# Optimization experiments

Measured on AMD Instinct MI355X. Metric: run time of the kernel, lower is better.

The kernel has to match this reference:

```python
import jax, jax.numpy as jnp
import numpy as np
from jax import lax

IN_FEATURES = 1024
NUM_TAGS = 128
C = NUM_TAGS + 3          # CRF adds start/stop (+1 pad slot per original code)
START_IDX = C - 2
STOP_IDX = C - 1
NEG = -10000.0


def setup_inputs() -> dict:
    key = jax.random.key(0)
    k1, k2, k3, k4 = jax.random.split(key, 4)
    B, L = 64, 512
    x = jax.random.normal(k1, (B, L, IN_FEATURES), dtype=jnp.float32)
    mask = jnp.ones((B, L), dtype=jnp.float32)
    W = jax.random.normal(k2, (C, IN_FEATURES), dtype=jnp.float32) * (1.0 / np.sqrt(IN_FEATURES))
    b = jax.random.normal(k3, (C,), dtype=jnp.float32) * 0.01
    transitions = jax.random.normal(k4, (C, C), dtype=jnp.float32)
    # transitions[i, j] = score of transitioning FROM j TO i
    transitions = transitions.at[START_IDX, :].set(NEG)   # never transition into start
    transitions = transitions.at[:, STOP_IDX].set(NEG)    # never transition out of stop
    return {"x": x, "mask": mask, "W": W, "b": b, "transitions": transitions}


def reference(x, mask, W, b, transitions):
    """CRF forward: linear projection + Viterbi decode.
    Returns (best_score [B], best_paths [B, L])."""
    feats = jnp.einsum("bld,cd->blc", x, W) + b          # [B, L, C]
    B, L, Cn = feats.shape

    init_score = jnp.full((B, Cn), NEG, dtype=feats.dtype).at[:, START_IDX].set(0.0)

    def viterbi_step(score, inp):
        feat_t, mask_t = inp                              # [B, C], [B]
        # acc[b, i, j] = score[b, j] + transitions[i, j]
        acc = score[:, None, :] + transitions[None, :, :]  # [B, C, C]
        best = jnp.max(acc, axis=-1)                      # [B, C]
        bp = jnp.argmax(acc, axis=-1).astype(jnp.int32)   # [B, C]
        m = mask_t[:, None]
        new_score = (best + feat_t) * m + score * (1.0 - m)
        return new_score, bp

    final_score, bps = lax.scan(
        viterbi_step, init_score,
        (jnp.transpose(feats, (1, 0, 2)), mask.T))        # bps: [L, B, C]

    final_score = final_score + transitions[STOP_IDX]     # [B, C]
    best_score = jnp.max(final_score, axis=-1)            # [B]
    best_tag = jnp.argmax(final_score, axis=-1).astype(jnp.int32)  # [B]

    def backtrack(tag, bp_t):
        # tag: current tag at timestep t; bp_t: [B, C] backpointers at t
        prev = jnp.take_along_axis(bp_t, tag[:, None], axis=1)[:, 0]
        return prev, tag                                  # emit tag at timestep t

    _, path = lax.scan(backtrack, best_tag, bps, reverse=True)  # path: [L, B]
    best_paths = path.T                                   # [B, L]
    return best_score, best_paths
```

## Files before the change

### kernel.cpp

```cpp
#include <hip/hip_runtime.h>

#define BB 64
#define LL 512
#define DD 1024
#define CC 131
#define CP 132
#define START_I 129
#define STOP_I 130
#define NEGV -10000.0f

__device__ __forceinline__ void lds_barrier() {
    asm volatile("s_waitcnt lgkmcnt(0)" ::: "memory");
    __builtin_amdgcn_s_barrier();
    __builtin_amdgcn_sched_barrier(0);
}

#define RL(src, i) __int_as_float(__builtin_amdgcn_readlane(__float_as_int(src), (i)))

#define GM 64
#define GK 32
#define LSTR 36

__global__ __launch_bounds__(256, 2) void gemm_feats(
    const float* __restrict__ x, const float* __restrict__ W,
    const float* __restrict__ bias, float* __restrict__ feats)
{
    __shared__ float xs[GM * LSTR];
    __shared__ float ws[CP * LSTR];

    const int tid = threadIdx.x;
    const int m0 = blockIdx.x * GM;
    const int tm = tid & 15;
    const int tj = (tid >> 4) & 15;
    const bool tail = (tj < 3);
    const int tjt = (tj < 3) ? tj : 2;

    float acc[4][8];
    float acct[4];
#pragma unroll
    for (int r = 0; r < 4; ++r) {
        acct[r] = 0.f;
#pragma unroll
        for (int c = 0; c < 8; ++c) acc[r][c] = 0.f;
    }

    for (int kc = 0; kc < DD / GK; ++kc) {
        const int k0 = kc * GK;
        if (kc) __syncthreads();
#pragma unroll
        for (int q = 0; q < 2; ++q) {
            int lin = tid + q * 256;
            int m = lin >> 3, c4 = lin & 7;
            float4 v = *(const float4*)&x[(size_t)(m0 + m) * DD + k0 + c4 * 4];
            *(float4*)&xs[m * LSTR + c4 * 4] = v;
        }
#pragma unroll
        for (int q = 0; q < 5; ++q) {
            int lin = tid + q * 256;
            if (lin < CC * 8) {
                int r = lin >> 3, c4 = lin & 7;
                float4 v = *(const float4*)&W[(size_t)r * DD + k0 + c4 * 4];
                *(float4*)&ws[r * LSTR + c4 * 4] = v;
            }
        }
        __syncthreads();

#pragma unroll
        for (int k4 = 0; k4 < 8; ++k4) {
            float4 xr[4], wr[8], wt;
#pragma unroll
            for (int r = 0; r < 4; ++r)
                xr[r] = *(const float4*)&xs[(tm + 16 * r) * LSTR + k4 * 4];
#pragma unroll
            for (int c = 0; c < 8; ++c)
                wr[c] = *(const float4*)&ws[(tj + 16 * c) * LSTR + k4 * 4];
            wt = *(const float4*)&ws[(128 + tjt) * LSTR + k4 * 4];
#pragma unroll
            for (int r = 0; r < 4; ++r) {
#pragma unroll
                for (int c = 0; c < 8; ++c) {
                    acc[r][c] = fmaf(xr[r].x, wr[c].x, acc[r][c]);
                    acc[r][c] = fmaf(xr[r].y, wr[c].y, acc[r][c]);
                    acc[r][c] = fmaf(xr[r].z, wr[c].z, acc[r][c]);
                    acc[r][c] = fmaf(xr[r].w, wr[c].w, acc[r][c]);
                }
                acct[r] = fmaf(xr[r].x, wt.x, acct[r]);
                acct[r] = fmaf(xr[r].y, wt.y, acct[r]);
                acct[r] = fmaf(xr[r].z, wt.z, acct[r]);
                acct[r] = fmaf(xr[r].w, wt.w, acct[r]);
            }
        }
    }

#pragma unroll
    for (int c = 0; c < 8; ++c) {
        int j = tj + 16 * c;
        float bv = bias[j];
#pragma unroll
        for (int r = 0; r < 4; ++r)
            feats[(size_t)(m0 + tm + 16 * r) * CP + j] = acc[r][c] + bv;
    }
    if (tail) {
        int j = 128 + tj;
        float bv = bias[j];
#pragma unroll
        for (int r = 0; r < 4; ++r)
            feats[(size_t)(m0 + tm + 16 * r) * CP + j] = acct[r] + bv;
    }
}

__global__ __launch_bounds__(192, 1) void viterbi_fwd(
    const float* __restrict__ feats, const float* __restrict__ mask,
    const float* __restrict__ trans, float* __restrict__ hist)
{
    const int b = blockIdx.x;
    const int tid = threadIdx.x;
    const int wave = tid >> 6, lane = tid & 63;
    const int colc = (wave < 2) ? (wave * 64 + lane)
                                : (128 + ((lane < 2) ? lane : 2));
    const bool owner = (wave < 2) || (lane < 3);

    __shared__ float sbuf[2][132];

    float4 T[33];
    {
        const float* tr = trans + (size_t)colc * CC;
#pragma unroll
        for (int q = 0; q < 32; ++q) {
            T[q].x = tr[4 * q + 0]; T[q].y = tr[4 * q + 1];
            T[q].z = tr[4 * q + 2]; T[q].w = tr[4 * q + 3];
        }
        T[32].x = tr[128]; T[32].y = tr[129]; T[32].z = tr[130];
        T[32].w = NEGV;
    }
#pragma unroll
    for (int q = 0; q < 33; ++q)
        asm volatile("" : "+v"(T[q].x), "+v"(T[q].y), "+v"(T[q].z), "+v"(T[q].w));

    for (int q = tid; q < 2 * 132; q += 192) {
        int bufi = q / 132, idx = q - bufi * 132;
        sbuf[bufi][idx] = (bufi == 0 && idx == START_I) ? 0.f : NEGV;
    }
    __syncthreads();

    const float* fb = feats + (size_t)b * LL * CP;
    const float* mb = mask + (size_t)b * LL;
    float* hb = hist + (size_t)b * LL * CP;

    float s_reg = (colc == START_I) ? 0.f : NEGV;

    float fv0 = fb[colc], fv1 = fb[CP + colc];
    float mv0 = mb[0], mv1 = mb[1];
    const float* fb_t = fb + 2 * CP + colc;
    const float* mb_t = mb + 2;
    float* hb_t = hb + colc;

    int cur = 0;
    float ns_p = 0.f;

    for (int t = 0; t < LL; ++t) {
        if (t > 0) {
            if (owner) *hb_t = ns_p;
            hb_t += CP;
        }
        float fv2 = 0.f, mv2 = 1.f;
        if (t + 2 < LL) { fv2 = *fb_t; mv2 = *mb_t; }
        fb_t += CP; ++mb_t;

        float sa = sbuf[cur][lane];
        float sb = sbuf[cur][64 + lane];
        float s128 = sbuf[cur][128], s129 = sbuf[cur][129], s130 = sbuf[cur][130];

        float a0 = -3.0e38f, a1 = -3.0e38f, a2 = -3.0e38f, a3 = -3.0e38f;
#pragma unroll
        for (int q = 0; q < 16; ++q) {
            float4 t4 = T[q];
            a0 = fmaxf(fmaxf(RL(sa, 4 * q + 0) + t4.x, RL(sa, 4 * q + 1) + t4.y), a0);
            a1 = fmaxf(fmaxf(RL(sa, 4 * q + 2) + t4.z, RL(sa, 4 * q + 3) + t4.w), a1);
        }
#pragma unroll
        for (int q = 0; q < 16; ++q) {
            float4 t4 = T[16 + q];
            a2 = fmaxf(fmaxf(RL(sb, 4 * q + 0) + t4.x, RL(sb, 4 * q + 1) + t4.y), a2);
            a3 = fmaxf(fmaxf(RL(sb, 4 * q + 2) + t4.z, RL(sb, 4 * q + 3) + t4.w), a3);
        }
        {
            float4 t4 = T[32];
            a0 = fmaxf(fmaxf(s128 + t4.x, s129 + t4.y), a0);
            a1 = fmaxf(a1, s130 + t4.z);
        }
        float best = fmaxf(fmaxf(a0, a1), fmaxf(a2, a3));

        float ns = (mv0 != 0.f) ? (best + fv0) : s_reg;
        s_reg = ns;
        if (owner) sbuf[cur ^ 1][colc] = ns;
        ns_p = ns;

        lds_barrier();

        fv0 = fv1; fv1 = fv2; mv0 = mv1; mv1 = mv2;
        cur ^= 1;
    }
    if (owner) *hb_t = ns_p;
}

__global__ __launch_bounds__(256, 4) void bp_kernel(
    const float* __restrict__ hist, const float* __restrict__ trans,
    unsigned char* __restrict__ bp)
{
    const int b  = blockIdx.x / 5;
    const int jc = blockIdx.x % 5;
    const int tc = blockIdx.y;
    const int tid = threadIdx.x;
    const int j0 = jc * 32;

    __shared__ float Ts[32][136];
    __shared__ float hs[8][132];

    for (int q = 0; q < 17; ++q) {
        int lin = tid + q * 256;
        if (lin < 32 * CC) {
            int r = lin / CC, i = lin - r * CC;
            if (j0 + r < CC) Ts[r][i] = trans[(size_t)(j0 + r) * CC + i];
        }
    }
    {
        const float4* src = (const float4*)(hist + ((size_t)b * LL + tc * 8) * CP);
#pragma unroll
        for (int q = 0; q < 2; ++q) {
            int lin = tid + q * 256;
            if (lin < (8 * CP) / 4) ((float4*)hs)[lin] = src[lin];
        }
    }
    __syncthreads();

    const int jl = tid & 31;
    const int tt = tid >> 5;
    const int j = j0 + jl;
    const int t = tc * 8 + tt + 1;
    if (j >= CC || t >= LL) return;

    float best; int idx;
    {
        float4 tv = *(const float4*)&Ts[jl][128];
        float4 hv = *(const float4*)&hs[tt][128];
        best = hv.z + tv.z; idx = 130;
        float v;
        v = hv.y + tv.y; if (v >= best) { best = v; idx = 129; }
        v = hv.x + tv.x; if (v >= best) { best = v; idx = 128; }
    }
#pragma unroll
    for (int i4 = 31; i4 >= 0; --i4) {
        float4 tv = *(const float4*)&Ts[jl][i4 * 4];
        float4 hv = *(const float4*)&hs[tt][i4 * 4];
        float v;
        v = hv.w + tv.w; if (v >= best) { best = v; idx = i4 * 4 + 3; }
        v = hv.z + tv.z; if (v >= best) { best = v; idx = i4 * 4 + 2; }
        v = hv.y + tv.y; if (v >= best) { best = v; idx = i4 * 4 + 1; }
        v = hv.x + tv.x; if (v >= best) { best = v; idx = i4 * 4 + 0; }
    }
    bp[((size_t)b * LL + t) * CP + j] = (unsigned char)idx;
}

__global__ __launch_bounds__(64, 1) void viterbi_btr(
    const float* __restrict__ hist, const float* __restrict__ trans,
    const unsigned char* __restrict__ bp,
    float* __restrict__ out_score, float* __restrict__ out_path)
{
    const int b = blockIdx.x;
    const int lane = threadIdx.x;
    const float* hb = hist + ((size_t)b * LL + (LL - 1)) * CP;
    const float* ts = trans + (size_t)STOP_I * CC;

    float v0 = hb[lane] + ts[lane];
    float v1 = hb[lane + 64] + ts[lane + 64];
    float v2 = (lane < 3) ? (hb[lane + 128] + ts[lane + 128]) : -3.0e38f;

    float best = v0; int idx = lane;
    if (v1 > best) { best = v1; idx = lane + 64; }
    if (v2 > best) { best = v2; idx = lane + 128; }
#pragma unroll
    for (int off = 32; off >= 1; off >>= 1) {
        float ob = __shfl_xor(best, off, 64);
        int   oi = __shfl_xor(idx, off, 64);
        if (ob > best || (ob == best && oi < idx)) { best = ob; idx = oi; }
    }

    float* op = out_path + (size_t)b * LL;
    if (lane == 0) {
        out_score[b] = best;
        op[LL - 1] = (float)idx;
    }
    int tag = idx;

    __shared__ unsigned char buf[2][1088];
    const unsigned char* bpb = bp + (size_t)b * LL * CP;

    {
        const unsigned int* src = (const unsigned int*)(bpb + (size_t)504 * CP);
        unsigned int* dst = (unsigned int*)buf[1];
#pragma unroll
        for (int q = 0; q < 5; ++q) {
            int lin = lane + q * 64;
            if (lin < 264) dst[lin] = src[lin];
        }
    }
    lds_barrier();

    int cur = 1;
    for (int k = 63; k >= 0; --k) {
        unsigned int r0 = 0, r1 = 0, r2 = 0, r3 = 0, r4 = 0;
        if (k > 0) {
            const unsigned int* src = (const unsigned int*)(bpb + (size_t)(k - 1) * 8 * CP);
            r0 = src[lane];
            r1 = src[lane + 64];
            r2 = src[lane + 128];
            r3 = src[lane + 192];
            if (lane < 8) r4 = src[lane + 256];
        }
        const unsigned char* cb = buf[cur];
#pragma unroll
        for (int s = 7; s >= 0; --s) {
            int t = k * 8 + s;
            if (t >= 1) {
                tag = cb[s * CP + tag];
                if (lane == 0) op[t - 1] = (float)tag;
            }
        }
        if (k > 0) {
            unsigned int* dst = (unsigned int*)buf[cur ^ 1];
            dst[lane] = r0;
            dst[lane + 64] = r1;
            dst[lane + 128] = r2;
            dst[lane + 192] = r3;
            if (lane < 8) dst[lane + 256] = r4;
            lds_barrier();
        }
        cur ^= 1;
    }
}

extern "C" void kernel_launch(void* const* d_in, const int* in_sizes, int n_in,
                              void* d_out, int out_size, void* d_ws, size_t ws_size,
                              hipStream_t stream)
{
    const float* x     = (const float*)d_in[0];
    const float* mask  = (const float*)d_in[1];
    const float* W     = (const float*)d_in[2];
    const float* bias  = (const float*)d_in[3];
    const float* trans = (const float*)d_in[4];

    float* feats = (float*)d_ws;
    float* hist  = feats + (size_t)BB * LL * CP;
    unsigned char* bp = (unsigned char*)(hist + (size_t)BB * LL * CP);
    float* out_score = (float*)d_out;
    float* out_path  = out_score + BB;

    hipLaunchKernelGGL(gemm_feats, dim3((BB * LL) / GM), dim3(256), 0, stream, x, W, bias, feats);
    hipLaunchKernelGGL(viterbi_fwd, dim3(BB), dim3(192), 0, stream, feats, mask, trans, hist);
    hipLaunchKernelGGL(bp_kernel, dim3(BB * 5, 64), dim3(256), 0, stream, hist, trans, bp);
    hipLaunchKernelGGL(viterbi_btr, dim3(BB), dim3(64), 0, stream, hist, trans, bp, out_score, out_path);
}
```

Baseline: 732.6 us.

## Split Viterbi forward max over source-state halves across four waves

```diff
diff --git a/kernel.cpp b/kernel.cpp
--- a/kernel.cpp
+++ b/kernel.cpp
@@ -109,99 +109,145 @@
     }
 }
 
-__global__ __launch_bounds__(192, 1) void viterbi_fwd(
+__global__ __launch_bounds__(256, 1) void viterbi_fwd(
     const float* __restrict__ feats, const float* __restrict__ mask,
     const float* __restrict__ trans, float* __restrict__ hist)
 {
     const int b = blockIdx.x;
     const int tid = threadIdx.x;
     const int wave = tid >> 6, lane = tid & 63;
-    const int colc = (wave < 2) ? (wave * 64 + lane)
-                                : (128 + ((lane < 2) ? lane : 2));
-    const bool owner = (wave < 2) || (lane < 3);
-
-    __shared__ float sbuf[2][132];
-
-    float4 T[33];
+    const int h  = wave >> 1;
+    const int jg = wave & 1;
+    const int j  = jg * 64 + lane;
+    const int c  = h * 64 + lane;
+
+    __shared__ float pbuf[2][2][132];
+    __shared__ float tpbuf[2][3][2];
+
+    float4 T[17];
     {
-        const float* tr = trans + (size_t)colc * CC;
-#pragma unroll
-        for (int q = 0; q < 32; ++q) {
+        const float* tr = trans + (size_t)j * CC + h * 64;
+#pragma unroll
+        for (int q = 0; q < 16; ++q) {
             T[q].x = tr[4 * q + 0]; T[q].y = tr[4 * q + 1];
             T[q].z = tr[4 * q + 2]; T[q].w = tr[4 * q + 3];
         }
-        T[32].x = tr[128]; T[32].y = tr[129]; T[32].z = tr[130];
-        T[32].w = NEGV;
-    }
-#pragma unroll
-    for (int q = 0; q < 33; ++q)
+        if (h == 0) {
+            T[16] = make_float4(NEGV, NEGV, NEGV, NEGV);
+        } else {
+            T[16].x = tr[64]; T[16].y = tr[65]; T[16].z = tr[66];
+            T[16].w = NEGV;
+        }
+    }
+#pragma unroll
+    for (int q = 0; q < 17; ++q)
         asm volatile("" : "+v"(T[q].x), "+v"(T[q].y), "+v"(T[q].z), "+v"(T[q].w));
 
-    for (int q = tid; q < 2 * 132; q += 192) {
-        int bufi = q / 132, idx = q - bufi * 132;
-        sbuf[bufi][idx] = (bufi == 0 && idx == START_I) ? 0.f : NEGV;
-    }
-    __syncthreads();
+    const int tjA = (jg == 0) ? 128 : 130;
+    const bool hasB = (jg == 0);
+    float ttA = trans[(size_t)tjA * CC + h * 64 + lane];
+    float ttB = hasB ? trans[(size_t)129 * CC + h * 64 + lane] : NEGV;
+    float ttxA = NEGV, ttxB = NEGV;
+    if (h == 1 && lane < 3) {
+        ttxA = trans[(size_t)tjA * CC + 128 + lane];
+        if (hasB) ttxB = trans[(size_t)129 * CC + 128 + lane];
+    }
 
     const float* fb = feats + (size_t)b * LL * CP;
     const float* mb = mask + (size_t)b * LL;
     float* hb = hist + (size_t)b * LL * CP;
 
-    float s_reg = (colc == START_I) ? 0.f : NEGV;
-
-    float fv0 = fb[colc], fv1 = fb[CP + colc];
+    float  sa = NEGV;
+    float4 sv = make_float4(NEGV, 0.f, NEGV, NEGV);
+    float  st = (lane == 1) ? 0.f : NEGV;
+
+    const bool tl = (h == 1 && lane < 3);
+
+    float fv0 = fb[c], fv1 = fb[CP + c];
     float mv0 = mb[0], mv1 = mb[1];
-    const float* fb_t = fb + 2 * CP + colc;
-    const float* mb_t = mb + 2;
-    float* hb_t = hb + colc;
+    float ft0 = 0.f, ft1 = 0.f;
+    if (tl) { ft0 = fb[128 + lane]; ft1 = fb[CP + 128 + lane]; }
+    const float* fb_t  = fb + 2 * CP + c;
+    const float* ftb_t = fb + 2 * CP + 128 + lane;
+    const float* mb_t  = mb + 2;
 
     int cur = 0;
-    float ns_p = 0.f;
-
     for (int t = 0; t < LL; ++t) {
-        if (t > 0) {
-            if (owner) *hb_t = ns_p;
-            hb_t += CP;
-        }
-        float fv2 = 0.f, mv2 = 1.f;
-        if (t + 2 < LL) { fv2 = *fb_t; mv2 = *mb_t; }
-        fb_t += CP; ++mb_t;
-
-        float sa = sbuf[cur][lane];
-        float sb = sbuf[cur][64 + lane];
-        float s128 = sbuf[cur][128], s129 = sbuf[cur][129], s130 = sbuf[cur][130];
+        float fv2 = 0.f, mv2 = 1.f, ft2 = 0.f;
+        if (t + 2 < LL) { fv2 = *fb_t; mv2 = *mb_t; if (tl) ft2 = *ftb_t; }
+        fb_t += CP; ftb_t += CP; ++mb_t;
 
         float a0 = -3.0e38f, a1 = -3.0e38f, a2 = -3.0e38f, a3 = -3.0e38f;
 #pragma unroll
-        for (int q = 0; q < 16; ++q) {
+        for (int q = 0; q < 8; ++q) {
             float4 t4 = T[q];
             a0 = fmaxf(fmaxf(RL(sa, 4 * q + 0) + t4.x, RL(sa, 4 * q + 1) + t4.y), a0);
             a1 = fmaxf(fmaxf(RL(sa, 4 * q + 2) + t4.z, RL(sa, 4 * q + 3) + t4.w), a1);
         }
 #pragma unroll
-        for (int q = 0; q < 16; ++q) {
-            float4 t4 = T[16 + q];
-            a2 = fmaxf(fmaxf(RL(sb, 4 * q + 0) + t4.x, RL(sb, 4 * q + 1) + t4.y), a2);
-            a3 = fmaxf(fmaxf(RL(sb, 4 * q + 2) + t4.z, RL(sb, 4 * q + 3) + t4.w), a3);
-        }
+        for (int q = 8; q < 16; ++q) {
+            float4 t4 = T[q];
+            a2 = fmaxf(fmaxf(RL(sa, 4 * q + 0) + t4.x, RL(sa, 4 * q + 1) + t4.y), a2);
+            a3 = fmaxf(fmaxf(RL(sa, 4 * q + 2) + t4.z, RL(sa, 4 * q + 3) + t4.w), a3);
+        }
+        if (h == 1) {
+            float4 t4 = T[16];
+            a0 = fmaxf(fmaxf(sv.x + t4.x, sv.y + t4.y), a0);
+            a1 = fmaxf(fmaxf(sv.z + t4.z, sv.w + t4.w), a1);
+        }
+        float p = fmaxf(fmaxf(a0, a1), fmaxf(a2, a3));
+        pbuf[cur][h][j] = p;
+
         {
-            float4 t4 = T[32];
-            a0 = fmaxf(fmaxf(s128 + t4.x, s129 + t4.y), a0);
-            a1 = fmaxf(a1, s130 + t4.z);
-        }
-        float best = fmaxf(fmaxf(a0, a1), fmaxf(a2, a3));
-
-        float ns = (mv0 != 0.f) ? (best + fv0) : s_reg;
-        s_reg = ns;
-        if (owner) sbuf[cur ^ 1][colc] = ns;
-        ns_p = ns;
+            float cA = sa + ttA;
+            if (h == 1 && lane < 3) {
+                float svl = (lane == 0) ? sv.x : ((lane == 1) ? sv.y : sv.z);
+                cA = fmaxf(cA, svl + ttxA);
+            }
+#pragma unroll
+            for (int off = 1; off < 64; off <<= 1)
+                cA = fmaxf(cA, __shfl_xor(cA, off, 64));
+            if (lane == 0) tpbuf[cur][tjA - 128][h] = cA;
+            if (hasB) {
+                float cB = sa + ttB;
+                if (h == 1 && lane < 3) {
+                    float svl = (lane == 0) ? sv.x : ((lane == 1) ? sv.y : sv.z);
+                    cB = fmaxf(cB, svl + ttxB);
+                }
+#pragma unroll
+                for (int off = 1; off < 64; off <<= 1)
+                    cB = fmaxf(cB, __shfl_xor(cB, off, 64));
+                if (lane == 0) tpbuf[cur][1][h] = cB;
+            }
+        }
 
         lds_barrier();
 
-        fv0 = fv1; fv1 = fv2; mv0 = mv1; mv1 = mv2;
+        {
+            float best = fmaxf(pbuf[cur][0][c], pbuf[cur][1][c]);
+            float ns = (mv0 != 0.f) ? (best + fv0) : sa;
+            sa = ns;
+            if (wave == 0 || wave == 2) hb[(size_t)t * CP + c] = ns;
+        }
+        if (h == 1) {
+            float2 u0 = *(const float2*)&tpbuf[cur][0][0];
+            float2 u1 = *(const float2*)&tpbuf[cur][1][0];
+            float2 u2 = *(const float2*)&tpbuf[cur][2][0];
+            float c128 = fmaxf(u0.x, u0.y);
+            float c129 = fmaxf(u1.x, u1.y);
+            float c130 = fmaxf(u2.x, u2.y);
+            if (lane < 3) {
+                float comb = (lane == 0) ? c128 : ((lane == 1) ? c129 : c130);
+                float nst = (mv0 != 0.f) ? (comb + ft0) : st;
+                st = nst;
+                if (wave == 3) hb[(size_t)t * CP + 128 + lane] = nst;
+            }
+            sv.x = RL(st, 0); sv.y = RL(st, 1); sv.z = RL(st, 2); sv.w = NEGV;
+        }
+
+        fv0 = fv1; fv1 = fv2; mv0 = mv1; mv1 = mv2; ft0 = ft1; ft1 = ft2;
         cur ^= 1;
     }
-    if (owner) *hb_t = ns_p;
 }
 
 __global__ __launch_bounds__(256, 4) void bp_kernel(
@@ -357,7 +403,7 @@
     float* out_path  = out_score + BB;
 
     hipLaunchKernelGGL(gemm_feats, dim3((BB * LL) / GM), dim3(256), 0, stream, x, W, bias, feats);
-    hipLaunchKernelGGL(viterbi_fwd, dim3(BB), dim3(192), 0, stream, feats, mask, trans, hist);
+    hipLaunchKernelGGL(viterbi_fwd, dim3(BB), dim3(256), 0, stream, feats, mask, trans, hist);
     hipLaunchKernelGGL(bp_kernel, dim3(BB * 5, 64), dim3(256), 0, stream, hist, trans, bp);
     hipLaunchKernelGGL(viterbi_btr, dim3(BB), dim3(64), 0, stream, hist, trans, bp, out_score, out_path);
 }
```

After: 833.0 us. +13.7%, slower.

## Split Viterbi forward max across four waves plus dedicated tail wave

Applied to the files above, without the earlier changes.

```diff
diff --git a/kernel.cpp b/kernel.cpp
--- a/kernel.cpp
+++ b/kernel.cpp
@@ -109,99 +109,190 @@
     }
 }
 
-__global__ __launch_bounds__(192, 1) void viterbi_fwd(
+__global__ __launch_bounds__(320, 1) void viterbi_fwd(
     const float* __restrict__ feats, const float* __restrict__ mask,
     const float* __restrict__ trans, float* __restrict__ hist)
 {
     const int b = blockIdx.x;
     const int tid = threadIdx.x;
     const int wave = tid >> 6, lane = tid & 63;
-    const int colc = (wave < 2) ? (wave * 64 + lane)
-                                : (128 + ((lane < 2) ? lane : 2));
-    const bool owner = (wave < 2) || (lane < 3);
-
-    __shared__ float sbuf[2][132];
-
-    float4 T[33];
-    {
-        const float* tr = trans + (size_t)colc * CC;
-#pragma unroll
-        for (int q = 0; q < 32; ++q) {
-            T[q].x = tr[4 * q + 0]; T[q].y = tr[4 * q + 1];
-            T[q].z = tr[4 * q + 2]; T[q].w = tr[4 * q + 3];
-        }
-        T[32].x = tr[128]; T[32].y = tr[129]; T[32].z = tr[130];
-        T[32].w = NEGV;
-    }
-#pragma unroll
-    for (int q = 0; q < 33; ++q)
-        asm volatile("" : "+v"(T[q].x), "+v"(T[q].y), "+v"(T[q].z), "+v"(T[q].w));
-
-    for (int q = tid; q < 2 * 132; q += 192) {
-        int bufi = q / 132, idx = q - bufi * 132;
-        sbuf[bufi][idx] = (bufi == 0 && idx == START_I) ? 0.f : NEGV;
-    }
-    __syncthreads();
+
+    __shared__ float pbuf[2][2][132];
+    __shared__ float tbuf[2][4];
 
     const float* fb = feats + (size_t)b * LL * CP;
     const float* mb = mask + (size_t)b * LL;
     float* hb = hist + (size_t)b * LL * CP;
 
-    float s_reg = (colc == START_I) ? 0.f : NEGV;
-
-    float fv0 = fb[colc], fv1 = fb[CP + colc];
-    float mv0 = mb[0], mv1 = mb[1];
-    const float* fb_t = fb + 2 * CP + colc;
-    const float* mb_t = mb + 2;
-    float* hb_t = hb + colc;
-
-    int cur = 0;
-    float ns_p = 0.f;
-
-    for (int t = 0; t < LL; ++t) {
-        if (t > 0) {
-            if (owner) *hb_t = ns_p;
+    if (wave < 4) {
+        const int h = wave >> 1;
+        const int jg = wave & 1;
+        const int j = jg * 64 + lane;
+        const int c = h * 64 + lane;
+        const bool hstore = (jg == 0);
+
+        float4 T[16];
+        float t16x = NEGV, t16y = NEGV, t16z = NEGV;
+        {
+            const float* tr = trans + (size_t)j * CC + h * 64;
+#pragma unroll
+            for (int q = 0; q < 16; ++q) {
+                T[q].x = tr[4 * q + 0]; T[q].y = tr[4 * q + 1];
+                T[q].z = tr[4 * q + 2]; T[q].w = tr[4 * q + 3];
+            }
+            if (h == 1) { t16x = tr[64]; t16y = tr[65]; t16z = tr[66]; }
+        }
+
+        if (wave == 0 && lane < 4)
+            tbuf[1][lane] = (128 + lane == START_I) ? 0.f : NEGV;
+        lds_barrier();
+
+        float sa = NEGV;
+
+#define MAIN_SCAN(TB, WB)                                                       \
+        {                                                                       \
+            float a0 = -3.0e38f, a1 = -3.0e38f, a2 = -3.0e38f, a3 = -3.0e38f;   \
+            _Pragma("unroll")                                                   \
+            for (int q = 0; q < 8; ++q) {                                       \
+                float4 t4 = T[q];                                               \
+                a0 = fmaxf(fmaxf(RL(sa, 4*q+0) + t4.x, RL(sa, 4*q+1) + t4.y), a0); \
+                a1 = fmaxf(fmaxf(RL(sa, 4*q+2) + t4.z, RL(sa, 4*q+3) + t4.w), a1); \
+            }                                                                   \
+            _Pragma("unroll")                                                   \
+            for (int q = 8; q < 16; ++q) {                                      \
+                float4 t4 = T[q];                                               \
+                a2 = fmaxf(fmaxf(RL(sa, 4*q+0) + t4.x, RL(sa, 4*q+1) + t4.y), a2); \
+                a3 = fmaxf(fmaxf(RL(sa, 4*q+2) + t4.z, RL(sa, 4*q+3) + t4.w), a3); \
+            }                                                                   \
+            if (h == 1) {                                                       \
+                float u0 = tbuf[TB][0], u1 = tbuf[TB][1], u2 = tbuf[TB][2];     \
+                a0 = fmaxf(fmaxf(u0 + t16x, u1 + t16y), a0);                    \
+                a1 = fmaxf(a1, u2 + t16z);                                      \
+            }                                                                   \
+            pbuf[WB][h][j] = fmaxf(fmaxf(a0, a1), fmaxf(a2, a3));               \
+        }
+
+        MAIN_SCAN(1, 0)
+        lds_barrier();
+
+        float fv0 = fb[c], fv1 = fb[CP + c];
+        float mv0 = mb[0], mv1 = mb[1];
+        const float* fb_t = fb + 2 * CP + c;
+        const float* mb_t = mb + 2;
+        float* hb_t = hb + c;
+
+        for (int t = 0; t < LL; ++t) {
+            const int rb = t & 1, wb = rb ^ 1;
+            float fv2 = 0.f, mv2 = 1.f;
+            if (t + 2 < LL) { fv2 = *fb_t; mv2 = *mb_t; }
+            fb_t += CP; ++mb_t;
+
+            float p0 = pbuf[rb][0][c], p1 = pbuf[rb][1][c];
+            float ns = (mv0 != 0.f) ? (fmaxf(p0, p1) + fv0) : sa;
+            sa = ns;
+            if (hstore) *hb_t = ns;
             hb_t += CP;
-        }
-        float fv2 = 0.f, mv2 = 1.f;
-        if (t + 2 < LL) { fv2 = *fb_t; mv2 = *mb_t; }
-        fb_t += CP; ++mb_t;
-
-        float sa = sbuf[cur][lane];
-        float sb = sbuf[cur][64 + lane];
-        float s128 = sbuf[cur][128], s129 = sbuf[cur][129], s130 = sbuf[cur][130];
-
-        float a0 = -3.0e38f, a1 = -3.0e38f, a2 = -3.0e38f, a3 = -3.0e38f;
-#pragma unroll
-        for (int q = 0; q < 16; ++q) {
-            float4 t4 = T[q];
-            a0 = fmaxf(fmaxf(RL(sa, 4 * q + 0) + t4.x, RL(sa, 4 * q + 1) + t4.y), a0);
-            a1 = fmaxf(fmaxf(RL(sa, 4 * q + 2) + t4.z, RL(sa, 4 * q + 3) + t4.w), a1);
-        }
-#pragma unroll
-        for (int q = 0; q < 16; ++q) {
-            float4 t4 = T[16 + q];
-            a2 = fmaxf(fmaxf(RL(sb, 4 * q + 0) + t4.x, RL(sb, 4 * q + 1) + t4.y), a2);
-            a3 = fmaxf(fmaxf(RL(sb, 4 * q + 2) + t4.z, RL(sb, 4 * q + 3) + t4.w), a3);
-        }
+
+            if (t < LL - 1) MAIN_SCAN(rb, wb)
+            lds_barrier();
+            fv0 = fv1; fv1 = fv2; mv0 = mv1; mv1 = mv2;
+        }
+#undef MAIN_SCAN
+    } else {
+        const int g = lane >> 4;
+        const int jt = (g < 3) ? g : 2;
+        const int ch = lane & 15;
+        const int i0 = ch * 9;
+        const bool wr = (lane < 48) && (ch == 0);
+        const int tj = 128 + jt;
+
+        float T9[9], sp[9];
+#pragma unroll
+        for (int k = 0; k < 9; ++k) {
+            int i = i0 + k;
+            T9[k] = (i < CC) ? trans[(size_t)tj * CC + i] : NEGV;
+            sp[k] = (i == START_I) ? 0.f : NEGV;
+        }
+        lds_barrier();
+
         {
-            float4 t4 = T[32];
-            a0 = fmaxf(fmaxf(s128 + t4.x, s129 + t4.y), a0);
-            a1 = fmaxf(a1, s130 + t4.z);
-        }
-        float best = fmaxf(fmaxf(a0, a1), fmaxf(a2, a3));
-
-        float ns = (mv0 != 0.f) ? (best + fv0) : s_reg;
-        s_reg = ns;
-        if (owner) sbuf[cur ^ 1][colc] = ns;
-        ns_p = ns;
-
-        lds_barrier();
-
-        fv0 = fv1; fv1 = fv2; mv0 = mv1; mv1 = mv2;
-        cur ^= 1;
-    }
-    if (owner) *hb_t = ns_p;
+            float m0v = mb[0];
+            float f0t = fb[tj];
+            float cd = -3.0e38f;
+#pragma unroll
+            for (int k = 0; k < 9; ++k) cd = fmaxf(cd, sp[k] + T9[k]);
+#pragma unroll
+            for (int off = 1; off < 16; off <<= 1)
+                cd = fmaxf(cd, __shfl_xor(cd, off, 64));
+            float st0 = (m0v != 0.f) ? (cd + f0t) : ((tj == START_I) ? 0.f : NEGV);
+            if (wr) { tbuf[0][jt] = st0; hb[tj] = st0; }
+            sp[0] = sp[0];
+            asm volatile("" ::: );
+            (void)st0;
+            __builtin_amdgcn_s_barrier();
+            asm volatile("s_waitcnt lgkmcnt(0)" ::: "memory");
+            __builtin_amdgcn_sched_barrier(0);
+
+            float st = st0;
+            float f9c[9], f9n[9];
+#pragma unroll
+            for (int k = 0; k < 9; ++k) {
+                int i = i0 + k;
+                f9c[k] = fb[(i < 128) ? i : 0];
+                f9n[k] = 0.f;
+            }
+            float ftc = fb[CP + tj];
+            float mv0_ = mb[0], mv1_ = mb[1];
+            const float* mb_t = mb + 2;
+            const float* fpn = fb + CP;
+            float* ht = hb + CP + tj;
+
+            for (int t = 0; t < LL; ++t) {
+                const int rb = t & 1, wb = rb ^ 1;
+                float mv2_ = 1.f, ftn = 0.f;
+                if (t + 2 < LL) { mv2_ = *mb_t; ftn = fpn[CP + tj]; }
+                ++mb_t;
+                if (t + 1 < LL) {
+#pragma unroll
+                    for (int k = 0; k < 9; ++k) {
+                        int i = i0 + k;
+                        f9n[k] = fpn[(i < 128) ? i : 0];
+                    }
+                }
+                fpn += CP;
+
+                float rl128 = RL(st, 0), rl129 = RL(st, 16), rl130 = RL(st, 32);
+#pragma unroll
+                for (int k = 0; k < 9; ++k) {
+                    int i = i0 + k;
+                    bool lt = (i < 128);
+                    int ic = lt ? i : 0;
+                    float pm = fmaxf(pbuf[rb][0][ic], pbuf[rb][1][ic]);
+                    float cmb = (mv0_ != 0.f) ? (pm + f9c[k]) : sp[k];
+                    float tv = (i == 128) ? rl128 :
+                               ((i == 129) ? rl129 : ((i == 130) ? rl130 : NEGV));
+                    sp[k] = lt ? cmb : tv;
+                }
+
+                if (t < LL - 1) {
+                    float cd = -3.0e38f;
+#pragma unroll
+                    for (int k = 0; k < 9; ++k) cd = fmaxf(cd, sp[k] + T9[k]);
+#pragma unroll
+                    for (int off = 1; off < 16; off <<= 1)
+                        cd = fmaxf(cd, __shfl_xor(cd, off, 64));
+                    float nst = (mv1_ != 0.f) ? (cd + ftc) : st;
+                    st = nst;
+                    if (wr) { tbuf[wb][jt] = nst; *ht = nst; }
+                }
+                ht += CP;
+                lds_barrier();
+                mv0_ = mv1_; mv1_ = mv2_; ftc = ftn;
+#pragma unroll
+                for (int k = 0; k < 9; ++k) f9c[k] = f9n[k];
+            }
+        }
+    }
 }
 
 __global__ __launch_bounds__(256, 4) void bp_kernel(
@@ -357,7 +448,7 @@
     float* out_path  = out_score + BB;
 
     hipLaunchKernelGGL(gemm_feats, dim3((BB * LL) / GM), dim3(256), 0, stream, x, W, bias, feats);
-    hipLaunchKernelGGL(viterbi_fwd, dim3(BB), dim3(192), 0, stream, feats, mask, trans, hist);
+    hipLaunchKernelGGL(viterbi_fwd, dim3(BB), dim3(320), 0, stream, feats, mask, trans, hist);
     hipLaunchKernelGGL(bp_kernel, dim3(BB * 5, 64), dim3(256), 0, stream, hist, trans, bp);
     hipLaunchKernelGGL(viterbi_btr, dim3(BB), dim3(64), 0, stream, hist, trans, bp, out_score, out_path);
 }
```

Measured after the change: 1.242 ms. 69.6% more time.

## Split Viterbi max-reduction across four waves using LDS float4 broadcast reads

Applied to the files above, without the earlier changes.

```diff
diff --git a/kernel.cpp b/kernel.cpp
--- a/kernel.cpp
+++ b/kernel.cpp
@@ -14,8 +14,6 @@
     __builtin_amdgcn_s_barrier();
     __builtin_amdgcn_sched_barrier(0);
 }
-
-#define RL(src, i) __int_as_float(__builtin_amdgcn_readlane(__float_as_int(src), (i)))
 
 #define GM 64
 #define GK 32
@@ -109,99 +107,130 @@
     }
 }
 
-__global__ __launch_bounds__(192, 1) void viterbi_fwd(
+__global__ __launch_bounds__(256, 1) void viterbi_fwd(
     const float* __restrict__ feats, const float* __restrict__ mask,
     const float* __restrict__ trans, float* __restrict__ hist)
 {
     const int b = blockIdx.x;
     const int tid = threadIdx.x;
-    const int wave = tid >> 6, lane = tid & 63;
-    const int colc = (wave < 2) ? (wave * 64 + lane)
-                                : (128 + ((lane < 2) ? lane : 2));
-    const bool owner = (wave < 2) || (lane < 3);
-
-    __shared__ float sbuf[2][132];
-
-    float4 T[33];
-    {
-        const float* tr = trans + (size_t)colc * CC;
-#pragma unroll
-        for (int q = 0; q < 32; ++q) {
-            T[q].x = tr[4 * q + 0]; T[q].y = tr[4 * q + 1];
-            T[q].z = tr[4 * q + 2]; T[q].w = tr[4 * q + 3];
-        }
-        T[32].x = tr[128]; T[32].y = tr[129]; T[32].z = tr[130];
-        T[32].w = NEGV;
-    }
-#pragma unroll
-    for (int q = 0; q < 33; ++q)
-        asm volatile("" : "+v"(T[q].x), "+v"(T[q].y), "+v"(T[q].z), "+v"(T[q].w));
-
-    for (int q = tid; q < 2 * 132; q += 192) {
-        int bufi = q / 132, idx = q - bufi * 132;
-        sbuf[bufi][idx] = (bufi == 0 && idx == START_I) ? 0.f : NEGV;
-    }
-    __syncthreads();
+    const int w = tid >> 6, lane = tid & 63;
+    const int h = w >> 1;
+    const int jg = w & 1;
+    const int j = jg * 64 + lane;
+    const bool cmb = (h == 0);
+
+    __shared__ float sbuf[2][136];
+    __shared__ float pbuf[2][2][128];
 
     const float* fb = feats + (size_t)b * LL * CP;
     const float* mb = mask + (size_t)b * LL;
     float* hb = hist + (size_t)b * LL * CP;
 
-    float s_reg = (colc == START_I) ? 0.f : NEGV;
-
-    float fv0 = fb[colc], fv1 = fb[CP + colc];
+    float4 T[17];
+    {
+        const float* tr = trans + (size_t)j * CC + h * 64;
+#pragma unroll
+        for (int q = 0; q < 16; ++q) {
+            T[q].x = tr[4 * q + 0]; T[q].y = tr[4 * q + 1];
+            T[q].z = tr[4 * q + 2]; T[q].w = tr[4 * q + 3];
+        }
+        if (h == 0) {
+            T[16] = make_float4(NEGV, NEGV, NEGV, NEGV);
+        } else {
+            T[16].x = tr[64]; T[16].y = tr[65]; T[16].z = tr[66];
+            T[16].w = NEGV;
+        }
+    }
+
+    const int ch = lane & 15;
+    const int g0 = lane >> 4;
+    const int gt = (g0 < 3) ? g0 : 2;
+    const int tj = 128 + gt;
+    const bool twr = (w == 2) && (g0 < 3) && (ch == 0);
+    float T9[9];
+    int ie[9];
+    if (w == 2) {
+#pragma unroll
+        for (int k = 0; k < 9; ++k) {
+            int i = ch * 9 + k;
+            ie[k] = (i < 132) ? i : 131;
+            T9[k] = (i < CC) ? trans[(size_t)tj * CC + i] : NEGV;
+        }
+    }
+
+    for (int q = tid; q < 2 * 136; q += 256) {
+        int bi = q / 136, idx = q - bi * 136;
+        sbuf[bi][idx] = (bi == 0 && idx == START_I) ? 0.f : NEGV;
+    }
+    __syncthreads();
+
     float mv0 = mb[0], mv1 = mb[1];
-    const float* fb_t = fb + 2 * CP + colc;
     const float* mb_t = mb + 2;
-    float* hb_t = hb + colc;
-
-    int cur = 0;
-    float ns_p = 0.f;
+    float s_prev = NEGV;
+    float fv0 = 0.f, fv1 = 0.f;
+    const float* fb_t = fb + 2 * CP + j;
+    if (cmb) { fv0 = fb[j]; fv1 = fb[CP + j]; }
+    float st = (tj == START_I) ? 0.f : NEGV;
+    float ft0 = 0.f, ft1 = 0.f;
+    const float* ftb = fb + 2 * CP + tj;
+    if (w == 2) { ft0 = fb[tj]; ft1 = fb[CP + tj]; }
+    float* hb_j = hb + j;
 
     for (int t = 0; t < LL; ++t) {
-        if (t > 0) {
-            if (owner) *hb_t = ns_p;
-            hb_t += CP;
-        }
-        float fv2 = 0.f, mv2 = 1.f;
-        if (t + 2 < LL) { fv2 = *fb_t; mv2 = *mb_t; }
-        fb_t += CP; ++mb_t;
-
-        float sa = sbuf[cur][lane];
-        float sb = sbuf[cur][64 + lane];
-        float s128 = sbuf[cur][128], s129 = sbuf[cur][129], s130 = sbuf[cur][130];
-
-        float a0 = -3.0e38f, a1 = -3.0e38f, a2 = -3.0e38f, a3 = -3.0e38f;
-#pragma unroll
-        for (int q = 0; q < 16; ++q) {
-            float4 t4 = T[q];
-            a0 = fmaxf(fmaxf(RL(sa, 4 * q + 0) + t4.x, RL(sa, 4 * q + 1) + t4.y), a0);
-            a1 = fmaxf(fmaxf(RL(sa, 4 * q + 2) + t4.z, RL(sa, 4 * q + 3) + t4.w), a1);
-        }
-#pragma unroll
-        for (int q = 0; q < 16; ++q) {
-            float4 t4 = T[16 + q];
-            a2 = fmaxf(fmaxf(RL(sb, 4 * q + 0) + t4.x, RL(sb, 4 * q + 1) + t4.y), a2);
-            a3 = fmaxf(fmaxf(RL(sb, 4 * q + 2) + t4.z, RL(sb, 4 * q + 3) + t4.w), a3);
-        }
+        const int rb = t & 1;
+
         {
-            float4 t4 = T[32];
-            a0 = fmaxf(fmaxf(s128 + t4.x, s129 + t4.y), a0);
-            a1 = fmaxf(a1, s130 + t4.z);
-        }
-        float best = fmaxf(fmaxf(a0, a1), fmaxf(a2, a3));
-
-        float ns = (mv0 != 0.f) ? (best + fv0) : s_reg;
-        s_reg = ns;
-        if (owner) sbuf[cur ^ 1][colc] = ns;
-        ns_p = ns;
+            const float4* s4 = (const float4*)&sbuf[rb][h * 64];
+            float a0 = -3.0e38f, a1 = -3.0e38f, a2 = -3.0e38f, a3 = -3.0e38f;
+#pragma unroll
+            for (int q = 0; q < 8; ++q) {
+                float4 sv = s4[q]; float4 t4 = T[q];
+                a0 = fmaxf(fmaxf(sv.x + t4.x, sv.y + t4.y), a0);
+                a1 = fmaxf(fmaxf(sv.z + t4.z, sv.w + t4.w), a1);
+            }
+#pragma unroll
+            for (int q = 8; q < 17; ++q) {
+                float4 sv = s4[q]; float4 t4 = T[q];
+                a2 = fmaxf(fmaxf(sv.x + t4.x, sv.y + t4.y), a2);
+                a3 = fmaxf(fmaxf(sv.z + t4.z, sv.w + t4.w), a3);
+            }
+            pbuf[rb][h][j] = fmaxf(fmaxf(a0, a1), fmaxf(a2, a3));
+        }
 
         lds_barrier();
 
-        fv0 = fv1; fv1 = fv2; mv0 = mv1; mv1 = mv2;
-        cur ^= 1;
-    }
-    if (owner) *hb_t = ns_p;
+        float fv2 = 0.f, ft2 = 0.f, mv2 = 1.f;
+        if (t + 2 < LL) mv2 = *mb_t;
+        ++mb_t;
+
+        if (cmb) {
+            if (t + 2 < LL) fv2 = *fb_t;
+            fb_t += CP;
+            float p = fmaxf(pbuf[rb][0][j], pbuf[rb][1][j]);
+            float ns = (mv0 != 0.f) ? (p + fv0) : s_prev;
+            s_prev = ns;
+            sbuf[rb ^ 1][j] = ns;
+            *hb_j = ns;
+        } else if (w == 2) {
+            if (t + 2 < LL) ft2 = *ftb;
+            ftb += CP;
+            float cd = -3.0e38f;
+#pragma unroll
+            for (int k = 0; k < 9; ++k)
+                cd = fmaxf(cd, sbuf[rb][ie[k]] + T9[k]);
+#pragma unroll
+            for (int off = 1; off < 16; off <<= 1)
+                cd = fmaxf(cd, __shfl_xor(cd, off, 64));
+            float ns = (mv0 != 0.f) ? (cd + ft0) : st;
+            st = ns;
+            if (twr) { sbuf[rb ^ 1][tj] = ns; hb[(size_t)t * CP + tj] = ns; }
+        }
+        hb_j += CP;
+
+        lds_barrier();
+
+        fv0 = fv1; fv1 = fv2; mv0 = mv1; mv1 = mv2; ft0 = ft1; ft1 = ft2;
+    }
 }
 
 __global__ __launch_bounds__(256, 4) void bp_kernel(
@@ -357,7 +386,7 @@
     float* out_path  = out_score + BB;
 
     hipLaunchKernelGGL(gemm_feats, dim3((BB * LL) / GM), dim3(256), 0, stream, x, W, bias, feats);
-    hipLaunchKernelGGL(viterbi_fwd, dim3(BB), dim3(192), 0, stream, feats, mask, trans, hist);
+    hipLaunchKernelGGL(viterbi_fwd, dim3(BB), dim3(256), 0, stream, feats, mask, trans, hist);
     hipLaunchKernelGGL(bp_kernel, dim3(BB * 5, 64), dim3(256), 0, stream, hist, trans, bp);
     hipLaunchKernelGGL(viterbi_btr, dim3(BB), dim3(64), 0, stream, hist, trans, bp, out_score, out_path);
 }
```

Result: slower. 773.5 us (+5.6%).
